# Kernel tuning notes

Measured on AMD Instinct MI355X. Metric: run time of the kernel, lower is better.

Reference implementation:

```python
import jax, jax.numpy as jnp
import numpy as np

N_NODES = 30000
N_EDGES = 480000
IN_FEAT = 256
OUT_FEAT = 256
N_RELS = 8
N_HEADS = 4
HEAD_DIM = OUT_FEAT // N_HEADS
LEAKY_SLOPE = 0.2


def setup_inputs() -> dict:
    key = jax.random.key(0)
    ks = jax.random.split(key, 8)
    inputs = jax.random.normal(ks[0], (N_NODES, IN_FEAT), dtype=jnp.float32)
    conv_weights = jax.random.normal(ks[1], (N_RELS, N_HEADS, IN_FEAT, HEAD_DIM), dtype=jnp.float32) * (1.0 / np.sqrt(IN_FEAT))
    attn_l = jax.random.normal(ks[2], (N_RELS, N_HEADS, HEAD_DIM), dtype=jnp.float32) * 0.1
    attn_r = jax.random.normal(ks[3], (N_RELS, N_HEADS, HEAD_DIM), dtype=jnp.float32) * 0.1
    h_bias = jax.random.normal(ks[4], (OUT_FEAT,), dtype=jnp.float32) * 0.02
    edge_src = jax.random.randint(ks[5], (N_EDGES,), 0, N_NODES, dtype=jnp.int32)
    edge_dst = jax.random.randint(ks[6], (N_EDGES,), 0, N_NODES, dtype=jnp.int32)
    edge_type = jax.random.randint(ks[7], (N_EDGES,), 0, N_RELS, dtype=jnp.int32)
    return {"inputs": inputs, "conv_weights": conv_weights, "attn_l": attn_l,
            "attn_r": attn_r, "h_bias": h_bias, "edge_src": edge_src,
            "edge_dst": edge_dst, "edge_type": edge_type}


def reference(inputs, conv_weights, attn_l, attn_r, h_bias, edge_src, edge_dst, edge_type):
    # Per-relation dense transform of all node features: [R, N, H, D]
    feat_all = jnp.einsum('ni,rhid->rnhd', inputs, conv_weights)
    # Gather transformed source/destination features per edge: [E, H, D]
    feat_src_e = feat_all[edge_type, edge_src]
    feat_dst_e = feat_all[edge_type, edge_dst]
    # Per-edge attention logits (relation-specific attn vectors): [E, H]
    el = jnp.sum(feat_src_e * attn_l[edge_type], axis=-1)
    er = jnp.sum(feat_dst_e * attn_r[edge_type], axis=-1)
    e = jax.nn.leaky_relu(el + er, negative_slope=LEAKY_SLOPE)
    # Segment softmax over incoming edges of each destination node
    m = jax.ops.segment_max(e, edge_dst, num_segments=N_NODES)  # [N, H]
    ex = jnp.exp(e - m[edge_dst])
    denom = jax.ops.segment_sum(ex, edge_dst, num_segments=N_NODES)  # [N, H]
    alpha = ex / denom[edge_dst]  # [E, H]
    # Attention-weighted aggregation of transformed source features
    h = jax.ops.segment_sum(alpha[..., None] * feat_src_e, edge_dst, num_segments=N_NODES)  # [N, H, D]
    h = h.reshape(N_NODES, OUT_FEAT) + h_bias
    # activation=None, self_loop=False, dropout=0.0 (eval) -> identity
    return h
```

## Files before the change

kernel.cpp:

```cpp
#include <hip/hip_runtime.h>
#include <hip/hip_bf16.h>

#define N_NODES 30000
#define NPAD    30208
#define N_EDGES 480000
#define N_RELS  8
#define NB_SCAN 118

typedef short bf16x8 __attribute__((ext_vector_type(8)));
typedef float f32x4  __attribute__((ext_vector_type(4)));

__device__ __forceinline__ unsigned short f2bf(float f) {
    unsigned u = __float_as_uint(f);
    u += 0x7fffu + ((u >> 16) & 1u);
    return (unsigned short)(u >> 16);
}
__device__ __forceinline__ float bf2f(unsigned short h) {
    return __uint_as_float(((unsigned)h) << 16);
}
__device__ __forceinline__ ushort2 pk2bf(float a, float b) {
    __hip_bfloat162 t = __float22bfloat162_rn(float2{a, b});
    union { __hip_bfloat162 h; ushort2 u; } cv; cv.h = t; return cv.u;
}

__device__ __forceinline__ void load_lds16(const void* g, void* l) {
    __builtin_amdgcn_global_load_lds(
        (const __attribute__((address_space(1))) unsigned int*)g,
        (__attribute__((address_space(3))) unsigned int*)l,
        16, 0, 0);
}

__global__ void prep_kernel(const float* __restrict__ x, unsigned short* __restrict__ xbf,
                            const float* __restrict__ cw, unsigned short* __restrict__ wt,
                            const int* __restrict__ edst, int* __restrict__ counts) {
    int b = blockIdx.x;
    if (b < 3776) {
        int t = b * 256 + threadIdx.x;
        int base = t * 8;
        int n = base >> 8;
        unsigned short h[8];
        if (n < N_NODES) {
            float4 a = *(const float4*)(x + base);
            float4 c = *(const float4*)(x + base + 4);
            h[0]=f2bf(a.x); h[1]=f2bf(a.y); h[2]=f2bf(a.z); h[3]=f2bf(a.w);
            h[4]=f2bf(c.x); h[5]=f2bf(c.y); h[6]=f2bf(c.z); h[7]=f2bf(c.w);
        } else {
            #pragma unroll
            for (int i = 0; i < 8; ++i) h[i] = 0;
        }
        uint4 o;
        o.x = (unsigned)h[0] | ((unsigned)h[1] << 16);
        o.y = (unsigned)h[2] | ((unsigned)h[3] << 16);
        o.z = (unsigned)h[4] | ((unsigned)h[5] << 16);
        o.w = (unsigned)h[6] | ((unsigned)h[7] << 16);
        *(uint4*)(xbf + base) = o;
    } else if (b < 5824) {
        int o = (b - 3776) * 256 + threadIdx.x;
        int i = o & 255;
        int c = (o >> 8) & 255;
        int r = o >> 16;
        float v = cw[(((size_t)r * 4 + (c >> 6)) * 256 + i) * 64 + (c & 63)];
        wt[o] = f2bf(v);
    } else {
        int e = (b - 5824) * 256 + threadIdx.x;
        if (e < N_EDGES) atomicAdd(&counts[edst[e]], 1);
    }
}

__global__ void scan1_kernel(const int* __restrict__ counts, int* __restrict__ locexcl,
                             int* __restrict__ bsum) {
    __shared__ int sm[256];
    int tid = threadIdx.x;
    int idx = blockIdx.x * 256 + tid;
    int v = (idx < N_NODES) ? counts[idx] : 0;
    sm[tid] = v;
    __syncthreads();
    for (int o = 1; o < 256; o <<= 1) {
        int t = (tid >= o) ? sm[tid - o] : 0;
        __syncthreads();
        sm[tid] += t;
        __syncthreads();
    }
    int incl = sm[tid];
    if (idx < N_NODES) locexcl[idx] = incl - v;
    if (tid == 255) bsum[blockIdx.x] = incl;
}

__global__ void scan2_kernel(const int* __restrict__ bsum, int* __restrict__ bpre) {
    __shared__ int sm[128];
    int tid = threadIdx.x;
    int v = (tid < NB_SCAN) ? bsum[tid] : 0;
    sm[tid] = v;
    __syncthreads();
    for (int o = 1; o < 128; o <<= 1) {
        int t = (tid >= o) ? sm[tid - o] : 0;
        __syncthreads();
        sm[tid] += t;
        __syncthreads();
    }
    if (tid < NB_SCAN) bpre[tid] = sm[tid] - v;
}

__global__ void scan3_kernel(const int* __restrict__ locexcl, const int* __restrict__ bpre,
                             int* __restrict__ offsets, int* __restrict__ cursor) {
    int idx = blockIdx.x * 256 + threadIdx.x;
    if (idx < N_NODES) {
        int o = bpre[blockIdx.x] + locexcl[idx];
        offsets[idx] = o;
        cursor[idx]  = o;
    }
    if (idx == 0) offsets[N_NODES] = N_EDGES;
}

__global__ void scatter_kernel(
    const int* __restrict__ esrc, const int* __restrict__ edst, const int* __restrict__ etyp,
    int* __restrict__ cursor, int* __restrict__ srcoff)
{
    int e = blockIdx.x * 256 + threadIdx.x;
    if (e >= N_EDGES) return;
    int s = esrc[e], d = edst[e], t = etyp[e];
    int p = atomicAdd(&cursor[d], 1);
    srcoff[p] = (t << 28) | (t * NPAD + s);
}

__global__ __launch_bounds__(256, 4) void gemm_kernel(
    const unsigned short* __restrict__ xbf,
    const unsigned short* __restrict__ wt,
    const float* __restrict__ attn_l,
    const float* __restrict__ attn_r,
    unsigned short* __restrict__ feat,
    float* __restrict__ projl,
    float* __restrict__ projr)
{
    __shared__ __align__(16) unsigned char smem[12288];

    const int tid  = threadIdx.x;
    const int lane = tid & 63;
    const int w    = tid >> 6;
    const int wm   = w >> 1;
    const int wn   = w & 1;
    const int quad = lane >> 4;
    const int l15  = lane & 15;

    const int bid  = blockIdx.x;
    const int work = (bid & 7) * 944 + (bid >> 3);
    const int mt   = work >> 4;
    const int r    = (work >> 1) & 7;
    const int nt   = work & 1;
    const int mbase = mt * 64;
    const int nbase = nt * 128;

    const unsigned short* Asrc = xbf + (size_t)mbase * 256;
    const unsigned short* Bsrc = wt + ((size_t)r * 256 + nbase) * 256;

    f32x4 acc[4][2] = {};

    const int srow = w * 16 + (lane >> 2);
    const int c0   = lane & 3;

    for (int k0 = 0; k0 < 256; k0 += 32) {
        {
            int c = c0 ^ ((srow >> 1) & 3);
            load_lds16(Asrc + (size_t)srow * 256 + k0 + c * 8, smem + w * 1024);
        }
        #pragma unroll
        for (int n = 0; n < 2; ++n) {
            int row = n * 64 + srow;
            int c   = c0 ^ ((row >> 1) & 3);
            load_lds16(Bsrc + (size_t)row * 256 + k0 + c * 8, smem + 4096 + (n * 256 + w * 64) * 16);
        }
        __syncthreads();

        bf16x8 xf[2], wf[4];
        #pragma unroll
        for (int j = 0; j < 2; ++j) {
            int rr = wm * 32 + j * 16 + l15;
            int cc = quad ^ ((rr >> 1) & 3);
            xf[j] = *(const bf16x8*)(smem + rr * 64 + cc * 16);
        }
        #pragma unroll
        for (int i = 0; i < 4; ++i) {
            int rr = wn * 64 + i * 16 + l15;
            int cc = quad ^ ((rr >> 1) & 3);
            wf[i] = *(const bf16x8*)(smem + 4096 + rr * 64 + cc * 16);
        }

        #pragma unroll
        for (int i = 0; i < 4; ++i)
            #pragma unroll
            for (int j = 0; j < 2; ++j)
                acc[i][j] = __builtin_amdgcn_mfma_f32_16x16x32_bf16(wf[i], xf[j], acc[i][j], 0, 0, 0);
        __syncthreads();
    }

    #pragma unroll
    for (int j = 0; j < 2; ++j) {
        int node = mbase + wm * 32 + j * 16 + l15;
        size_t rowb = ((size_t)r * NPAD + node) * 256 + nbase + wn * 64;
        #pragma unroll
        for (int i = 0; i < 4; ++i) {
            ushort2 lo = pk2bf(acc[i][j][0], acc[i][j][1]);
            ushort2 hi = pk2bf(acc[i][j][2], acc[i][j][3]);
            ushort4 v;
            v.x = lo.x; v.y = lo.y; v.z = hi.x; v.w = hi.y;
            *(ushort4*)(feat + rowb + i * 16 + quad * 4) = v;
        }
    }

    const int head = nt * 2 + wn;
    float alv[4][4], arv[4][4];
    #pragma unroll
    for (int i = 0; i < 4; ++i)
        #pragma unroll
        for (int e = 0; e < 4; ++e) {
            int c = i * 16 + quad * 4 + e;
            alv[i][e] = attn_l[((size_t)r * 4 + head) * 64 + c];
            arv[i][e] = attn_r[((size_t)r * 4 + head) * 64 + c];
        }
    float* bufL = (float*)smem + w * 160;
    float* bufR = (float*)(smem + 4096) + w * 160;
    #pragma unroll
    for (int j = 0; j < 2; ++j) {
        float s1 = 0.f, s2 = 0.f;
        #pragma unroll
        for (int i = 0; i < 4; ++i)
            #pragma unroll
            for (int e = 0; e < 4; ++e) {
                s1 += acc[i][j][e] * alv[i][e];
                s2 += acc[i][j][e] * arv[i][e];
            }
        int node = j * 16 + l15;
        bufL[node * 5 + quad] = s1;
        bufR[node * 5 + quad] = s2;
    }
    if (lane < 32) {
        float sL = 0.f, sR = 0.f;
        #pragma unroll
        for (int q = 0; q < 4; ++q) { sL += bufL[lane * 5 + q]; sR += bufR[lane * 5 + q]; }
        int g = mbase + wm * 32 + lane;
        projl[((size_t)r * NPAD + g) * 4 + head] = sL;
        projr[((size_t)r * NPAD + g) * 4 + head] = sR;
    }
}

__global__ __launch_bounds__(256) void aggregate_kernel(
    const int* __restrict__ offsets, const int* __restrict__ srcoff,
    const float* __restrict__ projl, const float* __restrict__ projr,
    const unsigned short* __restrict__ feat,
    const float* __restrict__ bias, float* __restrict__ out)
{
    __shared__ float sm[2][64][5];
    int wid  = threadIdx.x >> 6;
    int slot = wid >> 1;
    int half = wid & 1;
    int v = blockIdx.x * 2 + slot;
    int lane = threadIdx.x & 63;
    int head = lane >> 4;
    int s0 = offsets[v], s1 = offsets[v + 1];
    int mid = s0 + ((s1 - s0 + 1) >> 1);
    int lo = half ? mid : s0;
    int hi = half ? s1  : mid;
    const int vb = v * 4 + head;
    float a0 = 0.f, a1 = 0.f, a2 = 0.f, a3 = 0.f, den = 0.f;
    int i = lo;
    for (; i + 8 <= hi; i += 8) {
        int so[8]; float pl[8], pr[8]; ushort4 ff[8];
        #pragma unroll
        for (int u = 0; u < 8; ++u) so[u] = srcoff[i + u];
        #pragma unroll
        for (int u = 0; u < 8; ++u) {
            int pidx = so[u] & 0x0FFFFFFF;
            pl[u] = projl[(size_t)pidx * 4 + head];
            pr[u] = projr[(size_t)(so[u] >> 28) * (NPAD * 4) + vb];
            ff[u] = *(const ushort4*)(feat + (size_t)pidx * 256 + lane * 4);
        }
        #pragma unroll
        for (int u = 0; u < 8; ++u) {
            float lv = pl[u] + pr[u];
            lv = lv > 0.f ? lv : 0.2f * lv;
            float ee = __expf(lv);
            den += ee;
            a0 += ee * bf2f(ff[u].x);
            a1 += ee * bf2f(ff[u].y);
            a2 += ee * bf2f(ff[u].z);
            a3 += ee * bf2f(ff[u].w);
        }
    }
    for (; i + 4 <= hi; i += 4) {
        int so[4]; float pl[4], pr[4]; ushort4 ff[4];
        #pragma unroll
        for (int u = 0; u < 4; ++u) so[u] = srcoff[i + u];
        #pragma unroll
        for (int u = 0; u < 4; ++u) {
            int pidx = so[u] & 0x0FFFFFFF;
            pl[u] = projl[(size_t)pidx * 4 + head];
            pr[u] = projr[(size_t)(so[u] >> 28) * (NPAD * 4) + vb];
            ff[u] = *(const ushort4*)(feat + (size_t)pidx * 256 + lane * 4);
        }
        #pragma unroll
        for (int u = 0; u < 4; ++u) {
            float lv = pl[u] + pr[u];
            lv = lv > 0.f ? lv : 0.2f * lv;
            float ee = __expf(lv);
            den += ee;
            a0 += ee * bf2f(ff[u].x);
            a1 += ee * bf2f(ff[u].y);
            a2 += ee * bf2f(ff[u].z);
            a3 += ee * bf2f(ff[u].w);
        }
    }
    for (; i < hi; ++i) {
        int so0 = srcoff[i];
        int pidx = so0 & 0x0FFFFFFF;
        float pl0 = projl[(size_t)pidx * 4 + head];
        float pr0 = projr[(size_t)(so0 >> 28) * (NPAD * 4) + vb];
        ushort4 f0 = *(const ushort4*)(feat + (size_t)pidx * 256 + lane * 4);
        float lv = pl0 + pr0;
        lv = lv > 0.f ? lv : 0.2f * lv;
        float ee = __expf(lv);
        den += ee;
        a0 += ee * bf2f(f0.x);
        a1 += ee * bf2f(f0.y);
        a2 += ee * bf2f(f0.z);
        a3 += ee * bf2f(f0.w);
    }
    if (half) {
        sm[slot][lane][0] = a0; sm[slot][lane][1] = a1;
        sm[slot][lane][2] = a2; sm[slot][lane][3] = a3;
        sm[slot][lane][4] = den;
    }
    __syncthreads();
    if (!half) {
        a0 += sm[slot][lane][0]; a1 += sm[slot][lane][1];
        a2 += sm[slot][lane][2]; a3 += sm[slot][lane][3];
        den += sm[slot][lane][4];
        float inv = den > 0.f ? 1.f / den : 0.f;
        float4 o;
        o.x = a0 * inv + bias[lane * 4 + 0];
        o.y = a1 * inv + bias[lane * 4 + 1];
        o.z = a2 * inv + bias[lane * 4 + 2];
        o.w = a3 * inv + bias[lane * 4 + 3];
        ((float4*)out)[(size_t)v * 64 + lane] = o;
    }
}

extern "C" void kernel_launch(void* const* d_in, const int* in_sizes, int n_in,
                              void* d_out, int out_size, void* d_ws, size_t ws_size,
                              hipStream_t stream) {
    const float* x    = (const float*)d_in[0];
    const float* cw   = (const float*)d_in[1];
    const float* al   = (const float*)d_in[2];
    const float* ar   = (const float*)d_in[3];
    const float* bias = (const float*)d_in[4];
    const int* esrc   = (const int*)d_in[5];
    const int* edst   = (const int*)d_in[6];
    const int* etyp   = (const int*)d_in[7];
    float* out        = (float*)d_out;

    char* ws = (char*)d_ws;
    size_t off = 0;
    auto alloc = [&](size_t bytes) { size_t o = off; off += (bytes + 255) & ~(size_t)255; return o; };

    unsigned short* xbf  = (unsigned short*)(ws + alloc((size_t)NPAD * 256 * 2));
    unsigned short* wt   = (unsigned short*)(ws + alloc((size_t)N_RELS * 256 * 256 * 2));
    unsigned short* feat = (unsigned short*)(ws + alloc((size_t)N_RELS * NPAD * 256 * 2));
    float* projl = (float*)(ws + alloc((size_t)N_RELS * NPAD * 4 * 4));
    float* projr = (float*)(ws + alloc((size_t)N_RELS * NPAD * 4 * 4));
    int* srcoff  = (int*)(ws + alloc((size_t)N_EDGES * 4));
    int* counts  = (int*)(ws + alloc((size_t)N_NODES * 4));
    int* offsets = (int*)(ws + alloc((size_t)(N_NODES + 1) * 4));
    int* cursor  = (int*)(ws + alloc((size_t)N_NODES * 4));
    int* locexcl = (int*)(ws + alloc((size_t)N_NODES * 4));
    int* bsum    = (int*)(ws + alloc((size_t)NB_SCAN * 4));
    int* bpre    = (int*)(ws + alloc((size_t)NB_SCAN * 4));

    hipMemsetAsync(counts, 0, (size_t)N_NODES * 4, stream);

    prep_kernel<<<7699, 256, 0, stream>>>(x, xbf, cw, wt, edst, counts);
    scan1_kernel<<<NB_SCAN, 256, 0, stream>>>(counts, locexcl, bsum);
    scan2_kernel<<<1, 128, 0, stream>>>(bsum, bpre);
    scan3_kernel<<<NB_SCAN, 256, 0, stream>>>(locexcl, bpre, offsets, cursor);
    scatter_kernel<<<1875, 256, 0, stream>>>(esrc, edst, etyp, cursor, srcoff);
    gemm_kernel<<<7552, 256, 0, stream>>>(xbf, wt, al, ar, feat, projl, projr);
    aggregate_kernel<<<15000, 256, 0, stream>>>(offsets, srcoff, projl, projr, feat, bias, out);
}
```

Baseline: 272.4 us.

## Enlarge GEMM tile to 128x128 and stage bf16 output through LDS

```diff
diff --git a/kernel.cpp b/kernel.cpp
--- a/kernel.cpp
+++ b/kernel.cpp
@@ -2,7 +2,7 @@
 #include <hip/hip_bf16.h>
 
 #define N_NODES 30000
-#define NPAD    30208
+#define NPAD    30080
 #define N_EDGES 480000
 #define N_RELS  8
 #define NB_SCAN 118
@@ -34,7 +34,7 @@
                             const float* __restrict__ cw, unsigned short* __restrict__ wt,
                             const int* __restrict__ edst, int* __restrict__ counts) {
     int b = blockIdx.x;
-    if (b < 3776) {
+    if (b < 3760) {
         int t = b * 256 + threadIdx.x;
         int base = t * 8;
         int n = base >> 8;
@@ -54,15 +54,15 @@
         o.z = (unsigned)h[4] | ((unsigned)h[5] << 16);
         o.w = (unsigned)h[6] | ((unsigned)h[7] << 16);
         *(uint4*)(xbf + base) = o;
-    } else if (b < 5824) {
-        int o = (b - 3776) * 256 + threadIdx.x;
+    } else if (b < 5808) {
+        int o = (b - 3760) * 256 + threadIdx.x;
         int i = o & 255;
         int c = (o >> 8) & 255;
         int r = o >> 16;
         float v = cw[(((size_t)r * 4 + (c >> 6)) * 256 + i) * 64 + (c & 63)];
         wt[o] = f2bf(v);
     } else {
-        int e = (b - 5824) * 256 + threadIdx.x;
+        int e = (b - 5808) * 256 + threadIdx.x;
         if (e < N_EDGES) atomicAdd(&counts[edst[e]], 1);
     }
 }
@@ -123,7 +123,7 @@
     srcoff[p] = (t << 28) | (t * NPAD + s);
 }
 
-__global__ __launch_bounds__(256, 4) void gemm_kernel(
+__global__ __launch_bounds__(256) void gemm_kernel(
     const unsigned short* __restrict__ xbf,
     const unsigned short* __restrict__ wt,
     const float* __restrict__ attn_l,
@@ -132,7 +132,7 @@
     float* __restrict__ projl,
     float* __restrict__ projr)
 {
-    __shared__ __align__(16) unsigned char smem[12288];
+    __shared__ __align__(16) unsigned char smem[36864];
 
     const int tid  = threadIdx.x;
     const int lane = tid & 63;
@@ -143,68 +143,56 @@
     const int l15  = lane & 15;
 
     const int bid  = blockIdx.x;
-    const int work = (bid & 7) * 944 + (bid >> 3);
+    const int work = (bid & 7) * 470 + (bid >> 3);
     const int mt   = work >> 4;
     const int r    = (work >> 1) & 7;
     const int nt   = work & 1;
-    const int mbase = mt * 64;
+    const int mbase = mt * 128;
     const int nbase = nt * 128;
 
     const unsigned short* Asrc = xbf + (size_t)mbase * 256;
     const unsigned short* Bsrc = wt + ((size_t)r * 256 + nbase) * 256;
 
-    f32x4 acc[4][2] = {};
+    f32x4 acc[4][4] = {};
 
     const int srow = w * 16 + (lane >> 2);
     const int c0   = lane & 3;
 
     for (int k0 = 0; k0 < 256; k0 += 32) {
-        {
-            int c = c0 ^ ((srow >> 1) & 3);
-            load_lds16(Asrc + (size_t)srow * 256 + k0 + c * 8, smem + w * 1024);
-        }
         #pragma unroll
         for (int n = 0; n < 2; ++n) {
             int row = n * 64 + srow;
             int c   = c0 ^ ((row >> 1) & 3);
-            load_lds16(Bsrc + (size_t)row * 256 + k0 + c * 8, smem + 4096 + (n * 256 + w * 64) * 16);
-        }
-        __syncthreads();
-
-        bf16x8 xf[2], wf[4];
-        #pragma unroll
-        for (int j = 0; j < 2; ++j) {
-            int rr = wm * 32 + j * 16 + l15;
-            int cc = quad ^ ((rr >> 1) & 3);
-            xf[j] = *(const bf16x8*)(smem + rr * 64 + cc * 16);
+            load_lds16(Asrc + (size_t)row * 256 + k0 + c * 8, smem + (n * 256 + w * 64) * 16);
+        }
+        #pragma unroll
+        for (int n = 0; n < 2; ++n) {
+            int row = n * 64 + srow;
+            int c   = c0 ^ ((row >> 1) & 3);
+            load_lds16(Bsrc + (size_t)row * 256 + k0 + c * 8, smem + 8192 + (n * 256 + w * 64) * 16);
+        }
+        __syncthreads();
+
+        bf16x8 xf[4], wf[4];
+        #pragma unroll
+        for (int j = 0; j < 4; ++j) {
+            int row = wm * 64 + j * 16 + l15;
+            int cc  = quad ^ ((row >> 1) & 3);
+            xf[j] = *(const bf16x8*)(smem + row * 64 + cc * 16);
         }
         #pragma unroll
         for (int i = 0; i < 4; ++i) {
-            int rr = wn * 64 + i * 16 + l15;
-            int cc = quad ^ ((rr >> 1) & 3);
-            wf[i] = *(const bf16x8*)(smem + 4096 + rr * 64 + cc * 16);
+            int row = wn * 64 + i * 16 + l15;
+            int cc  = quad ^ ((row >> 1) & 3);
+            wf[i] = *(const bf16x8*)(smem + 8192 + row * 64 + cc * 16);
         }
 
         #pragma unroll
         for (int i = 0; i < 4; ++i)
             #pragma unroll
-            for (int j = 0; j < 2; ++j)
+            for (int j = 0; j < 4; ++j)
                 acc[i][j] = __builtin_amdgcn_mfma_f32_16x16x32_bf16(wf[i], xf[j], acc[i][j], 0, 0, 0);
         __syncthreads();
-    }
-
-    #pragma unroll
-    for (int j = 0; j < 2; ++j) {
-        int node = mbase + wm * 32 + j * 16 + l15;
-        size_t rowb = ((size_t)r * NPAD + node) * 256 + nbase + wn * 64;
-        #pragma unroll
-        for (int i = 0; i < 4; ++i) {
-            ushort2 lo = pk2bf(acc[i][j][0], acc[i][j][1]);
-            ushort2 hi = pk2bf(acc[i][j][2], acc[i][j][3]);
-            ushort4 v;
-            v.x = lo.x; v.y = lo.y; v.z = hi.x; v.w = hi.y;
-            *(ushort4*)(feat + rowb + i * 16 + quad * 4) = v;
-        }
     }
 
     const int head = nt * 2 + wn;
@@ -217,10 +205,10 @@
             alv[i][e] = attn_l[((size_t)r * 4 + head) * 64 + c];
             arv[i][e] = attn_r[((size_t)r * 4 + head) * 64 + c];
         }
-    float* bufL = (float*)smem + w * 160;
-    float* bufR = (float*)(smem + 4096) + w * 160;
+    float* bufL = (float*)smem + w * 320;
+    float* bufR = (float*)(smem + 8192) + w * 320;
     #pragma unroll
-    for (int j = 0; j < 2; ++j) {
+    for (int j = 0; j < 4; ++j) {
         float s1 = 0.f, s2 = 0.f;
         #pragma unroll
         for (int i = 0; i < 4; ++i)
@@ -233,13 +221,40 @@
         bufL[node * 5 + quad] = s1;
         bufR[node * 5 + quad] = s2;
     }
-    if (lane < 32) {
-        float sL = 0.f, sR = 0.f;
-        #pragma unroll
-        for (int q = 0; q < 4; ++q) { sL += bufL[lane * 5 + q]; sR += bufR[lane * 5 + q]; }
-        int g = mbase + wm * 32 + lane;
-        projl[((size_t)r * NPAD + g) * 4 + head] = sL;
-        projr[((size_t)r * NPAD + g) * 4 + head] = sR;
+    float sL = 0.f, sR = 0.f;
+    #pragma unroll
+    for (int q = 0; q < 4; ++q) {
+        sL += bufL[lane * 5 + q];
+        sR += bufR[lane * 5 + q];
+    }
+    int g = mbase + wm * 64 + lane;
+    projl[((size_t)r * NPAD + g) * 4 + head] = sL;
+    projr[((size_t)r * NPAD + g) * 4 + head] = sR;
+
+    __syncthreads();
+
+    unsigned char* bb = smem + w * 8704;
+    #pragma unroll
+    for (int j = 0; j < 4; ++j) {
+        int rr = j * 16 + l15;
+        #pragma unroll
+        for (int i = 0; i < 4; ++i) {
+            ushort2 lo = pk2bf(acc[i][j][0], acc[i][j][1]);
+            ushort2 hi = pk2bf(acc[i][j][2], acc[i][j][3]);
+            uint2 v;
+            v.x = (unsigned)lo.x | ((unsigned)lo.y << 16);
+            v.y = (unsigned)hi.x | ((unsigned)hi.y << 16);
+            *(uint2*)(bb + rr * 136 + i * 32 + quad * 8) = v;
+        }
+    }
+    asm volatile("s_waitcnt lgkmcnt(0)" ::: "memory");
+    #pragma unroll
+    for (int q = 0; q < 8; ++q) {
+        int rr = q * 8 + (lane >> 3);
+        int c  = lane & 7;
+        uint4 v = *(const uint4*)(bb + rr * 136 + c * 16);
+        int node = mbase + wm * 64 + rr;
+        *(uint4*)(feat + ((size_t)r * NPAD + node) * 256 + nbase + wn * 64 + c * 8) = v;
     }
 }
 
@@ -376,11 +391,11 @@
 
     hipMemsetAsync(counts, 0, (size_t)N_NODES * 4, stream);
 
-    prep_kernel<<<7699, 256, 0, stream>>>(x, xbf, cw, wt, edst, counts);
+    prep_kernel<<<7683, 256, 0, stream>>>(x, xbf, cw, wt, edst, counts);
     scan1_kernel<<<NB_SCAN, 256, 0, stream>>>(counts, locexcl, bsum);
     scan2_kernel<<<1, 128, 0, stream>>>(bsum, bpre);
     scan3_kernel<<<NB_SCAN, 256, 0, stream>>>(locexcl, bpre, offsets, cursor);
     scatter_kernel<<<1875, 256, 0, stream>>>(esrc, edst, etyp, cursor, srcoff);
-    gemm_kernel<<<7552, 256, 0, stream>>>(xbf, wt, al, ar, feat, projl, projr);
+    gemm_kernel<<<3760, 256, 0, stream>>>(xbf, wt, al, ar, feat, projl, projr);
     aggregate_kernel<<<15000, 256, 0, stream>>>(offsets, srcoff, projl, projr, feat, bias, out);
 }
```

Measured after the change: 252.5 us. 1.08x faster.
